# Performance work log

Hardware: AMD Instinct MI355X
Metric: run time of the kernel (lower is better)

The kernel has to match this reference:

```python
import jax, jax.numpy as jnp
import numpy as np


def _gelu(x):
    # tf.nn.gelu default is exact (erf) gelu
    return jax.nn.gelu(x, approximate=False)


def _reduce_gat(x, W, A):
    # x: [..., n, f]; W: [f, d]; A: [2d, 1]
    wx = x @ W                                   # [..., n, d]
    root = jnp.broadcast_to(wx[..., 0:1, :], wx.shape)  # gather idx 0 + repeat
    cat = jnp.concatenate([wx, root], axis=-1)   # [..., n, 2d]
    z = _gelu(cat @ A)                           # Dense(1, activation=gelu)
    att = jax.nn.softmax(_gelu(z), axis=-2)      # gelu applied twice, then softmax over n
    return _gelu(jnp.sum(wx * att, axis=-2))     # [..., d]


def _layer(x, W, A):
    # W: [H, f, d], A: [H, 2d, 1]; mean over heads
    heads = jax.vmap(lambda w, a: _reduce_gat(x, w, a))(W, A)
    return jnp.mean(heads, axis=0)


def setup_inputs() -> dict:
    key = jax.random.key(0)
    k = jax.random.split(key, 5)
    B, N2, N1, F, D, H = 512, 16, 16, 256, 256, 4
    x = jax.random.normal(k[0], (B, N2, N1, F), dtype=jnp.float32)
    W0 = jax.random.normal(k[1], (H, F, D), dtype=jnp.float32) * 0.05
    A0 = jax.random.normal(k[2], (H, 2 * D, 1), dtype=jnp.float32) * 0.05
    W1 = jax.random.normal(k[3], (H, D, D), dtype=jnp.float32) * 0.05
    A1 = jax.random.normal(k[4], (H, 2 * D, 1), dtype=jnp.float32) * 0.05
    return {"x": x, "W0": W0, "A0": A0, "W1": W1, "A1": A1}


def reference(x, W0, A0, W1, A1):
    x = _layer(x, W0, A0)  # [B, N2, D]
    x = _layer(x, W1, A1)  # [B, D]
    return x
```

## Files before the change

kernel.cpp:

```cpp
#include <hip/hip_runtime.h>
#include <math.h>

typedef _Float16 half_t;
typedef __attribute__((ext_vector_type(8))) _Float16 half8;
typedef __attribute__((ext_vector_type(16))) float floatx16;

__device__ __forceinline__ float gelu_exact(float v) {
    return 0.5f * v * (1.0f + erff(v * 0.7071067811865476f));
}

__device__ __forceinline__ floatx16 zero16() {
    floatx16 z;
#pragma unroll
    for (int i = 0; i < 16; ++i) z[i] = 0.f;
    return z;
}

__device__ __forceinline__ int swz(int b) { return b ^ (((b >> 9) & 7) << 4); }

template <bool SWZ>
__device__ __forceinline__ half8 lds_frag(const half_t* p, int byteoff) {
    if (SWZ) byteoff = swz(byteoff);
    return *(const half8*)((const char*)p + byteoff);
}

#define MFMA16(a, b, c) __builtin_amdgcn_mfma_f32_32x32x16_f16((a), (b), (c), 0, 0, 0)

__global__ __launch_bounds__(256) void prep(const float* __restrict__ W0,
                                            const float* __restrict__ A0,
                                            const float* __restrict__ W1,
                                            const float* __restrict__ A1,
                                            half_t* __restrict__ Wsw0, half_t* __restrict__ Wsw1,
                                            half_t* __restrict__ Zah0, half_t* __restrict__ Zal0,
                                            half_t* __restrict__ Zah1, half_t* __restrict__ Zal1) {
    __shared__ float tile[32][257];
    const int t  = threadIdx.x;
    const int kb = blockIdx.x & 7;
    const int h  = (blockIdx.x >> 3) & 3;
    const int tz = blockIdx.x >> 5;
    const float* W = tz ? W1 : W0;
    const float* A = tz ? A1 : A0;
    half_t* Wsw = tz ? Wsw1 : Wsw0;
    half_t* Zh  = tz ? Zah1 : Zah0;
    half_t* Zl  = tz ? Zal1 : Zal0;

    for (int i = 0; i < 32; ++i)
        tile[i][t] = W[(size_t)(h * 256 + kb * 32 + i) * 256 + t];
    __syncthreads();

    const int j = t >> 5, lmn = t & 31;
#pragma unroll
    for (int i0 = 0; i0 < 32; i0 += 8) {
        const int ks = 2 * kb + (i0 >> 4);
        const int qq = (i0 >> 3) & 1;
        half_t hb[8];
#pragma unroll
        for (int ii = 0; ii < 8; ++ii) hb[ii] = (half_t)tile[i0 + ii][t];
        size_t off = ((size_t)(h * 16 + ks) * 8 + j) * 512 + (size_t)(32 * qq + lmn) * 8;
        *(half8*)&Wsw[off] = *(half8*)hb;
    }

    if (kb == 0) {
        const float4* Wr = (const float4*)&W[(size_t)(h * 256 + t) * 256];
        const float4* Al = (const float4*)&A[h * 512];
        const float4* Ah = (const float4*)&A[h * 512 + 256];
        float wl = 0.f, wh = 0.f;
        for (int d = 0; d < 64; ++d) {
            float4 wv = Wr[d], a0 = Al[d], a1 = Ah[d];
            wl += wv.x * a0.x + wv.y * a0.y + wv.z * a0.z + wv.w * a0.w;
            wh += wv.x * a1.x + wv.y * a1.y + wv.z * a1.z + wv.w * a1.w;
        }
        half_t hi = (half_t)wl;
        Zh[(2 * h) * 256 + t] = hi;
        Zl[(2 * h) * 256 + t] = (half_t)(wl - (float)hi);
        hi = (half_t)wh;
        Zh[(2 * h + 1) * 256 + t] = hi;
        Zl[(2 * h + 1) * 256 + t] = (half_t)(wh - (float)hi);
        if (h == 0) {
            for (int c = 8; c < 32; ++c) {
                Zh[c * 256 + t] = (half_t)0.f;
                Zl[c * 256 + t] = (half_t)0.f;
            }
        }
    }
}

template <int GROUPS>
__global__ __launch_bounds__(256, 2) void gat_layer(
    const float* __restrict__ x,
    const half_t* __restrict__ Wsw,
    const half_t* __restrict__ Zah, const half_t* __restrict__ Zal,
    float* __restrict__ out) {
    constexpr int ROWS = GROUPS * 16;
    constexpr int MT   = ROWS / 32;

    __shared__ half_t xsh[MT * 16 * 512];
    __shared__ half_t xsl[MT * 16 * 512];
    __shared__ float zlo_s[4][ROWS];
    __shared__ float zhi_s[4][ROWS];
    __shared__ float ge_s[4][ROWS];
    __shared__ float att_s[4][ROWS];

    const int t  = threadIdx.x;
    const int w  = t >> 6;
    const int l  = t & 63;
    const int lm = t & 31;
    const int q  = (t >> 5) & 1;

    {
        const float4* xg = (const float4*)(x + (size_t)blockIdx.x * ROWS * 256);
#pragma unroll
        for (int i = 0; i < ROWS / 8; ++i) {
            int e = t + 256 * i;
            int row = e >> 5, cc = e & 31;
            float4 v0 = xg[row * 64 + 2 * cc];
            float4 v1 = xg[row * 64 + 2 * cc + 1];
            half_t hb[8], lb[8];
            const float* vf = &v0.x;
#pragma unroll
            for (int ii = 0; ii < 8; ++ii) {
                float v = (ii < 4) ? vf[ii] : (&v1.x)[ii - 4];
                half_t hv = (half_t)v;
                hb[ii] = hv;
                lb[ii] = (half_t)(v - (float)hv);
            }
            int m = row >> 5, r31 = row & 31, ks = cc >> 1, kq = cc & 1;
            int base = ((m * 16 + ks) * 64 + 32 * kq + r31) * 8;
            *(half8*)&xsh[base] = *(half8*)hb;
            *(half8*)&xsl[base] = *(half8*)lb;
        }
    }
    __syncthreads();

    if (w == 0) {
        floatx16 zm[MT], zc[MT];
#pragma unroll
        for (int mt = 0; mt < MT; ++mt) { zm[mt] = zero16(); zc[mt] = zero16(); }
#pragma unroll 4
        for (int ks = 0; ks < 16; ++ks) {
            const int ko = lm * 256 + 16 * ks + 8 * q;
            half8 bh = *(const half8*)&Zah[ko];
            half8 bl = *(const half8*)&Zal[ko];
#pragma unroll
            for (int mt = 0; mt < MT; ++mt) {
                half8 a  = *(const half8*)&xsh[((mt * 16 + ks) * 64 + l) * 8];
                half8 al = *(const half8*)&xsl[((mt * 16 + ks) * 64 + l) * 8];
                zm[mt] = MFMA16(a, bh, zm[mt]);
                zc[mt] = MFMA16(al, bh, zc[mt]);
                zc[mt] = MFMA16(a, bl, zc[mt]);
            }
        }
        if (lm < 8) {
            int h = lm >> 1;
            float* dst = (lm & 1) ? &zhi_s[h][0] : &zlo_s[h][0];
#pragma unroll
            for (int mt = 0; mt < MT; ++mt)
#pragma unroll
                for (int r = 0; r < 16; ++r) {
                    int row = 32 * mt + 4 * q + (r & 3) + 8 * (r >> 2);
                    dst[row] = zm[mt][r] + zc[mt][r];
                }
        }
    }
    __syncthreads();

    {
        int h = t >> 6, r = t & 63;
        if (r < ROWS) {
            float z = zlo_s[h][r] + zhi_s[h][r & ~15];
            ge_s[h][r] = gelu_exact(gelu_exact(z));
        }
    }
    __syncthreads();
    {
        int h = t >> 6, r = t & 63;
        if (r < ROWS) {
            int g0 = r & ~15;
            float mx = -1e30f;
#pragma unroll
            for (int i = 0; i < 16; ++i) mx = fmaxf(mx, ge_s[h][g0 + i]);
            float s = 0.f;
#pragma unroll
            for (int i = 0; i < 16; ++i) s += expf(ge_s[h][g0 + i] - mx);
            att_s[h][r] = expf(ge_s[h][r] - mx) / s;
        }
    }
    __syncthreads();

    float outp[2][GROUPS];
#pragma unroll
    for (int nt = 0; nt < 2; ++nt)
#pragma unroll
        for (int g = 0; g < GROUPS; ++g) outp[nt][g] = 0.f;

#pragma unroll 1
    for (int h = 0; h < 4; ++h) {
        float tp[2][GROUPS];
#pragma unroll
        for (int nt = 0; nt < 2; ++nt)
#pragma unroll
            for (int g = 0; g < GROUPS; ++g) tp[nt][g] = 0.f;

        const half_t* Bp = Wsw + ((size_t)(h * 16) * 8 + 2 * w) * 512 + (size_t)l * 8;

#pragma unroll 1
        for (int pass = 0; pass < 2; ++pass) {
            const half_t* Xp = pass ? xsl : xsh;
            floatx16 acc[MT][2];
#pragma unroll
            for (int mt = 0; mt < MT; ++mt) { acc[mt][0] = zero16(); acc[mt][1] = zero16(); }

#pragma unroll
            for (int ks = 0; ks < 16; ++ks) {
                half8 b0 = *(const half8*)(Bp + (size_t)ks * 4096);
                half8 b1 = *(const half8*)(Bp + (size_t)ks * 4096 + 512);
#pragma unroll
                for (int mt = 0; mt < MT; ++mt) {
                    half8 a = *(const half8*)&Xp[((mt * 16 + ks) * 64 + l) * 8];
                    acc[mt][0] = MFMA16(a, b0, acc[mt][0]);
                    acc[mt][1] = MFMA16(a, b1, acc[mt][1]);
                }
            }

#pragma unroll
            for (int mt = 0; mt < MT; ++mt)
#pragma unroll
                for (int k = 0; k < 4; ++k) {
                    float4 a4 = *(const float4*)&att_s[h][32 * mt + 4 * q + 8 * k];
#pragma unroll
                    for (int jj = 0; jj < 4; ++jj) {
                        int r = 4 * k + jj;
                        int row = 32 * mt + 4 * q + 8 * k + jj;
                        int g = row >> 4;
                        float av = (&a4.x)[jj];
                        tp[0][g] = fmaf(acc[mt][0][r], av, tp[0][g]);
                        tp[1][g] = fmaf(acc[mt][1][r], av, tp[1][g]);
                    }
                }
        }

#pragma unroll
        for (int nt = 0; nt < 2; ++nt)
#pragma unroll
            for (int g = 0; g < GROUPS; ++g) {
                float s = tp[nt][g] + __shfl_xor(tp[nt][g], 32, 64);
                outp[nt][g] += gelu_exact(s);
            }
    }

    if (q == 0) {
#pragma unroll
        for (int g = 0; g < GROUPS; ++g) {
            size_t ro = ((size_t)blockIdx.x * GROUPS + g) * 256 + 64 * w;
            out[ro + lm]      = 0.25f * outp[0][g];
            out[ro + 32 + lm] = 0.25f * outp[1][g];
        }
    }
}


__device__ __forceinline__ void stage_chunk(const float4* __restrict__ xg,
                                            half_t* __restrict__ xsh,
                                            half_t* __restrict__ xsl, int e) {
    int row = e >> 5, cc = e & 31;
    float4 v0 = xg[row * 64 + 2 * cc];
    float4 v1 = xg[row * 64 + 2 * cc + 1];
    half_t hb[8], lb[8];
#pragma unroll
    for (int ii = 0; ii < 8; ++ii) {
        float v = (ii < 4) ? (&v0.x)[ii] : (&v1.x)[ii - 4];
        half_t hv = (half_t)v;
        hb[ii] = hv;
        lb[ii] = (half_t)(v - (float)hv);
    }
    int base = ((cc >> 1) * 64 + 32 * (cc & 1) + row) * 16;
    *(half8*)((char*)xsh + swz(base)) = *(half8*)hb;
    *(half8*)((char*)xsl + swz(base)) = *(half8*)lb;
}

__device__ __forceinline__ void z_phase(const half_t* __restrict__ xsh,
                                        const half_t* __restrict__ xsl,
                                        const half_t* __restrict__ Zah,
                                        const half_t* __restrict__ Zal,
                                        float* __restrict__ zrow,
                                        int w, int l, int lm, int q) {
    floatx16 zp = zero16();
#pragma unroll
    for (int kk = 0; kk < 4; ++kk) {
        int ks = 4 * w + kk;
        int ko = lm * 256 + 16 * ks + 8 * q;
        half8 bh = *(const half8*)&Zah[ko];
        half8 bl = *(const half8*)&Zal[ko];
        int ao = (ks * 64 + l) * 16;
        half8 ah = lds_frag<true>(xsh, ao);
        half8 al = lds_frag<true>(xsl, ao);
        zp = MFMA16(ah, bh, zp);
        zp = MFMA16(al, bh, zp);
        zp = MFMA16(ah, bl, zp);
    }
    if (lm < 8) {
#pragma unroll
        for (int r = 0; r < 16; ++r) {
            int row = 4 * q + (r & 3) + 8 * (r >> 2);
            zrow[row * 9 + lm] = zp[r];
        }
    }
}

__global__ __launch_bounds__(512, 1) void gat2(
    const float* __restrict__ y1, const half_t* __restrict__ Wsw,
    const half_t* __restrict__ Zah, const half_t* __restrict__ Zal,
    float* __restrict__ out) {
    __shared__ __align__(16) half_t xsh[16 * 512];
    __shared__ __align__(16) half_t xsl[16 * 512];
    __shared__ float zpart[4][32][9];
    __shared__ __align__(16) float ge_s[4][32];
    __shared__ __align__(16) float att_s[4][32];
    __shared__ float outp_s[4][2][256];

    const int t = threadIdx.x;
    const int w = t >> 6, l = t & 63, lm = t & 31, q = (t >> 5) & 1;

    const float4* xg = (const float4*)(y1 + (size_t)blockIdx.x * 32 * 256);
    stage_chunk(xg, xsh, xsl, t);
    stage_chunk(xg, xsh, xsl, t + 512);
    __syncthreads();

    if (w < 4) z_phase(xsh, xsl, Zah, Zal, &zpart[w][0][0], w, l, lm, q);
    __syncthreads();

    if (t < 128) {
        int h = t >> 5, r = t & 31;
        int c0 = 2 * h, c1 = 2 * h + 1, rr = r & ~15;
        float own  = zpart[0][r][c0] + zpart[1][r][c0] + zpart[2][r][c0] + zpart[3][r][c0];
        float root = zpart[0][rr][c1] + zpart[1][rr][c1] + zpart[2][rr][c1] + zpart[3][rr][c1];
        ge_s[h][r] = gelu_exact(gelu_exact(own + root));
    }
    __syncthreads();
    if (t < 128) {
        int h = t >> 5, r = t & 31;
        int g0 = r & ~15;
        float mx = -1e30f;
#pragma unroll
        for (int i = 0; i < 16; ++i) mx = fmaxf(mx, ge_s[h][g0 + i]);
        float sum = 0.f;
#pragma unroll
        for (int i = 0; i < 16; ++i) sum += expf(ge_s[h][g0 + i] - mx);
        att_s[h][r] = expf(ge_s[h][r] - mx) / sum;
    }
    __syncthreads();

    const int h = w >> 1, s = w & 1;
    const half_t* Bp = Wsw + ((size_t)(h * 16) * 8 + 4 * s) * 512 + (size_t)l * 8;

    float tp[4][2];
#pragma unroll
    for (int jc = 0; jc < 4; ++jc) { tp[jc][0] = 0.f; tp[jc][1] = 0.f; }

#pragma unroll 1
    for (int pass = 0; pass < 2; ++pass) {
        const half_t* Xp = pass ? xsl : xsh;
        floatx16 acc[4];
#pragma unroll
        for (int jc = 0; jc < 4; ++jc) acc[jc] = zero16();
#pragma unroll
        for (int ks = 0; ks < 16; ++ks) {
            int ao = (ks * 64 + l) * 16;
            half8 a = lds_frag<true>(Xp, ao);
#pragma unroll
            for (int jc = 0; jc < 4; ++jc) {
                half8 b = *(const half8*)(Bp + (size_t)ks * 4096 + jc * 512);
                acc[jc] = MFMA16(a, b, acc[jc]);
            }
        }
#pragma unroll
        for (int g = 0; g < 2; ++g)
#pragma unroll
            for (int k2 = 0; k2 < 2; ++k2)
#pragma unroll
                for (int jj = 0; jj < 4; ++jj) {
                    float av = att_s[h][16 * g + 8 * k2 + 4 * q + jj];
                    int r = jj + 4 * k2 + 8 * g;
#pragma unroll
                    for (int jc = 0; jc < 4; ++jc)
                        tp[jc][g] = fmaf(acc[jc][r], av, tp[jc][g]);
                }
    }

#pragma unroll
    for (int g = 0; g < 2; ++g)
#pragma unroll
        for (int jc = 0; jc < 4; ++jc) {
            float sf = tp[jc][g] + __shfl_xor(tp[jc][g], 32, 64);
            if (q == 0) outp_s[h][g][128 * s + 32 * jc + lm] = gelu_exact(sf);
        }
    __syncthreads();

    {
        int g = t >> 8, col = t & 255;
        float sm = outp_s[0][g][col] + outp_s[1][g][col] + outp_s[2][g][col] + outp_s[3][g][col];
        out[((size_t)blockIdx.x * 2 + g) * 256 + col] = 0.25f * sm;
    }
}

extern "C" void kernel_launch(void* const* d_in, const int* in_sizes, int n_in,
                              void* d_out, int out_size, void* d_ws, size_t ws_size,
                              hipStream_t stream) {
    const float* x  = (const float*)d_in[0];
    const float* W0 = (const float*)d_in[1];
    const float* A0 = (const float*)d_in[2];
    const float* W1 = (const float*)d_in[3];
    const float* A1 = (const float*)d_in[4];

    char* ws = (char*)d_ws;
    float*  y1   = (float*)ws;
    half_t* Wsw0 = (half_t*)(ws + 8388608);
    half_t* Wsw1 = (half_t*)(ws + 8912896);
    half_t* Zah0 = (half_t*)(ws + 9437184);
    half_t* Zal0 = (half_t*)(ws + 9453568);
    half_t* Zah1 = (half_t*)(ws + 9469952);
    half_t* Zal1 = (half_t*)(ws + 9486336);

    prep<<<64, 256, 0, stream>>>(W0, A0, W1, A1, Wsw0, Wsw1, Zah0, Zal0, Zah1, Zal1);
    gat_layer<4><<<2048, 256, 0, stream>>>(x, Wsw0, Zah0, Zal0, y1);
    gat2<<<256, 512, 0, stream>>>(y1, Wsw1, Zah1, Zal1, (float*)d_out);
}
```

Measured before the change: 372.9 us.

## Split layer-1 across two kernels and widen gat2 to 1024 threads

Adds a gat1m kernel that processes 64 rows per block with two M-tiles, so each W fragment loaded from global memory is reused across two MFMA row tiles. Layer-1 work is split evenly: half the blocks still run the existing gat_layer kernel and half run the new one, launched back to back. gat2 now uses 1024 threads, with each wave covering a narrower N strip and doing both the high and low fp16 passes in one loop instead of two sequential passes. The aim is more reuse of weight fragments and more parallelism per block, at the cost of higher register pressure and an extra kernel launch.

```diff
diff --git a/kernel.cpp b/kernel.cpp
--- a/kernel.cpp
+++ b/kernel.cpp
@@ -18,10 +18,8 @@
 
 __device__ __forceinline__ int swz(int b) { return b ^ (((b >> 9) & 7) << 4); }
 
-template <bool SWZ>
-__device__ __forceinline__ half8 lds_frag(const half_t* p, int byteoff) {
-    if (SWZ) byteoff = swz(byteoff);
-    return *(const half8*)((const char*)p + byteoff);
+__device__ __forceinline__ half8 lds_swz(const half_t* p, int byteoff) {
+    return *(const half8*)((const char*)p + swz(byteoff));
 }
 
 #define MFMA16(a, b, c) __builtin_amdgcn_mfma_f32_32x32x16_f16((a), (b), (c), 0, 0, 0)
@@ -273,41 +271,160 @@
         hb[ii] = hv;
         lb[ii] = (half_t)(v - (float)hv);
     }
-    int base = ((cc >> 1) * 64 + 32 * (cc & 1) + row) * 16;
+    int m = row >> 5, r31 = row & 31, ks = cc >> 1, kq = cc & 1;
+    int base = ((m * 16 + ks) * 64 + 32 * kq + r31) * 16;
     *(half8*)((char*)xsh + swz(base)) = *(half8*)hb;
     *(half8*)((char*)xsl + swz(base)) = *(half8*)lb;
 }
 
+template <int MT>
 __device__ __forceinline__ void z_phase(const half_t* __restrict__ xsh,
                                         const half_t* __restrict__ xsl,
                                         const half_t* __restrict__ Zah,
                                         const half_t* __restrict__ Zal,
                                         float* __restrict__ zrow,
                                         int w, int l, int lm, int q) {
-    floatx16 zp = zero16();
+    floatx16 zp[MT];
+#pragma unroll
+    for (int mt = 0; mt < MT; ++mt) zp[mt] = zero16();
 #pragma unroll
     for (int kk = 0; kk < 4; ++kk) {
         int ks = 4 * w + kk;
         int ko = lm * 256 + 16 * ks + 8 * q;
         half8 bh = *(const half8*)&Zah[ko];
         half8 bl = *(const half8*)&Zal[ko];
-        int ao = (ks * 64 + l) * 16;
-        half8 ah = lds_frag<true>(xsh, ao);
-        half8 al = lds_frag<true>(xsl, ao);
-        zp = MFMA16(ah, bh, zp);
-        zp = MFMA16(al, bh, zp);
-        zp = MFMA16(ah, bl, zp);
+#pragma unroll
+        for (int mt = 0; mt < MT; ++mt) {
+            int ao = ((mt * 16 + ks) * 64 + l) * 16;
+            half8 ah = lds_swz(xsh, ao);
+            half8 al = lds_swz(xsl, ao);
+            zp[mt] = MFMA16(ah, bh, zp[mt]);
+            zp[mt] = MFMA16(al, bh, zp[mt]);
+            zp[mt] = MFMA16(ah, bl, zp[mt]);
+        }
     }
     if (lm < 8) {
 #pragma unroll
-        for (int r = 0; r < 16; ++r) {
-            int row = 4 * q + (r & 3) + 8 * (r >> 2);
-            zrow[row * 9 + lm] = zp[r];
-        }
-    }
-}
-
-__global__ __launch_bounds__(512, 1) void gat2(
+        for (int mt = 0; mt < MT; ++mt)
+#pragma unroll
+            for (int r = 0; r < 16; ++r) {
+                int row = 32 * mt + 4 * q + (r & 3) + 8 * (r >> 2);
+                zrow[row * 9 + lm] = zp[mt][r];
+            }
+    }
+}
+
+__global__ __launch_bounds__(256, 2) void gat1m(
+    const float* __restrict__ x, const half_t* __restrict__ Wsw,
+    const half_t* __restrict__ Zah, const half_t* __restrict__ Zal,
+    float* __restrict__ out) {
+    __shared__ __align__(16) half_t xsh[32 * 512];
+    __shared__ __align__(16) half_t xsl[32 * 512];
+    __shared__ float zpart[4][64][9];
+    __shared__ __align__(16) float ge_s[4][64];
+    __shared__ __align__(16) float att_s[4][64];
+
+    const int t = threadIdx.x;
+    const int w = t >> 6, l = t & 63, lm = t & 31, q = (t >> 5) & 1;
+
+    const float4* xg = (const float4*)(x + (size_t)blockIdx.x * 64 * 256);
+#pragma unroll
+    for (int i = 0; i < 8; ++i) stage_chunk(xg, xsh, xsl, t + 256 * i);
+    __syncthreads();
+
+    z_phase<2>(xsh, xsl, Zah, Zal, &zpart[w][0][0], w, l, lm, q);
+    __syncthreads();
+
+    {
+        int h = t >> 6, r = t & 63;
+        int c0 = 2 * h, c1 = 2 * h + 1, rr = r & ~15;
+        float own  = zpart[0][r][c0] + zpart[1][r][c0] + zpart[2][r][c0] + zpart[3][r][c0];
+        float root = zpart[0][rr][c1] + zpart[1][rr][c1] + zpart[2][rr][c1] + zpart[3][rr][c1];
+        ge_s[h][r] = gelu_exact(gelu_exact(own + root));
+    }
+    __syncthreads();
+    {
+        int h = t >> 6, r = t & 63;
+        int g0 = r & ~15;
+        float mx = -1e30f;
+#pragma unroll
+        for (int i = 0; i < 16; ++i) mx = fmaxf(mx, ge_s[h][g0 + i]);
+        float sum = 0.f;
+#pragma unroll
+        for (int i = 0; i < 16; ++i) sum += expf(ge_s[h][g0 + i] - mx);
+        att_s[h][r] = expf(ge_s[h][r] - mx) / sum;
+    }
+    __syncthreads();
+
+    float outp[2][4];
+#pragma unroll
+    for (int nt = 0; nt < 2; ++nt)
+#pragma unroll
+        for (int g = 0; g < 4; ++g) outp[nt][g] = 0.f;
+
+#pragma unroll 1
+    for (int h = 0; h < 4; ++h) {
+        const half_t* Bp = Wsw + ((size_t)(h * 16) * 8 + 2 * w) * 512 + (size_t)l * 8;
+        floatx16 acc[2][2];
+        acc[0][0] = zero16(); acc[0][1] = zero16();
+        acc[1][0] = zero16(); acc[1][1] = zero16();
+#pragma unroll
+        for (int ks = 0; ks < 16; ++ks) {
+            half8 b0 = *(const half8*)(Bp + (size_t)ks * 4096);
+            half8 b1 = *(const half8*)(Bp + (size_t)ks * 4096 + 512);
+#pragma unroll
+            for (int mt = 0; mt < 2; ++mt) {
+                int ao = ((mt * 16 + ks) * 64 + l) * 16;
+                half8 ah = lds_swz(xsh, ao);
+                half8 al = lds_swz(xsl, ao);
+                acc[mt][0] = MFMA16(ah, b0, acc[mt][0]);
+                acc[mt][0] = MFMA16(al, b0, acc[mt][0]);
+                acc[mt][1] = MFMA16(ah, b1, acc[mt][1]);
+                acc[mt][1] = MFMA16(al, b1, acc[mt][1]);
+            }
+        }
+
+        float tp[2][4];
+#pragma unroll
+        for (int nt = 0; nt < 2; ++nt)
+#pragma unroll
+            for (int g = 0; g < 4; ++g) tp[nt][g] = 0.f;
+#pragma unroll
+        for (int mt = 0; mt < 2; ++mt)
+#pragma unroll
+            for (int k2 = 0; k2 < 2; ++k2)
+#pragma unroll
+                for (int kk = 0; kk < 2; ++kk)
+#pragma unroll
+                    for (int jj = 0; jj < 4; ++jj) {
+                        const int k = 2 * k2 + kk;
+                        const int r = 4 * k + jj;
+                        const int g = 2 * mt + k2;
+                        float av = att_s[h][32 * mt + 8 * k + 4 * q + jj];
+                        tp[0][g] = fmaf(acc[mt][0][r], av, tp[0][g]);
+                        tp[1][g] = fmaf(acc[mt][1][r], av, tp[1][g]);
+                    }
+
+#pragma unroll
+        for (int nt = 0; nt < 2; ++nt)
+#pragma unroll
+            for (int g = 0; g < 4; ++g) {
+                float s = tp[nt][g] + __shfl_xor(tp[nt][g], 32, 64);
+                outp[nt][g] += gelu_exact(s);
+            }
+    }
+
+    if (q == 0) {
+#pragma unroll
+        for (int g = 0; g < 4; ++g) {
+            size_t ro = ((size_t)blockIdx.x * 4 + g) * 256 + 64 * w;
+            out[ro + lm]      = 0.25f * outp[0][g];
+            out[ro + 32 + lm] = 0.25f * outp[1][g];
+        }
+    }
+}
+
+__global__ __launch_bounds__(1024, 1) void gat2(
     const float* __restrict__ y1, const half_t* __restrict__ Wsw,
     const half_t* __restrict__ Zah, const half_t* __restrict__ Zal,
     float* __restrict__ out) {
@@ -323,10 +440,9 @@
 
     const float4* xg = (const float4*)(y1 + (size_t)blockIdx.x * 32 * 256);
     stage_chunk(xg, xsh, xsl, t);
-    stage_chunk(xg, xsh, xsl, t + 512);
-    __syncthreads();
-
-    if (w < 4) z_phase(xsh, xsl, Zah, Zal, &zpart[w][0][0], w, l, lm, q);
+    __syncthreads();
+
+    if (w < 4) z_phase<1>(xsh, xsl, Zah, Zal, &zpart[w][0][0], w, l, lm, q);
     __syncthreads();
 
     if (t < 128) {
@@ -350,56 +466,50 @@
     }
     __syncthreads();
 
-    const int h = w >> 1, s = w & 1;
-    const half_t* Bp = Wsw + ((size_t)(h * 16) * 8 + 4 * s) * 512 + (size_t)l * 8;
-
-    float tp[4][2];
-#pragma unroll
-    for (int jc = 0; jc < 4; ++jc) { tp[jc][0] = 0.f; tp[jc][1] = 0.f; }
-
-#pragma unroll 1
-    for (int pass = 0; pass < 2; ++pass) {
-        const half_t* Xp = pass ? xsl : xsh;
-        floatx16 acc[4];
-#pragma unroll
-        for (int jc = 0; jc < 4; ++jc) acc[jc] = zero16();
-#pragma unroll
-        for (int ks = 0; ks < 16; ++ks) {
-            int ao = (ks * 64 + l) * 16;
-            half8 a = lds_frag<true>(Xp, ao);
-#pragma unroll
-            for (int jc = 0; jc < 4; ++jc) {
-                half8 b = *(const half8*)(Bp + (size_t)ks * 4096 + jc * 512);
-                acc[jc] = MFMA16(a, b, acc[jc]);
-            }
-        }
-#pragma unroll
-        for (int g = 0; g < 2; ++g)
-#pragma unroll
-            for (int k2 = 0; k2 < 2; ++k2)
-#pragma unroll
-                for (int jj = 0; jj < 4; ++jj) {
-                    float av = att_s[h][16 * g + 8 * k2 + 4 * q + jj];
-                    int r = jj + 4 * k2 + 8 * g;
-#pragma unroll
-                    for (int jc = 0; jc < 4; ++jc)
-                        tp[jc][g] = fmaf(acc[jc][r], av, tp[jc][g]);
-                }
-    }
-
-#pragma unroll
-    for (int g = 0; g < 2; ++g)
-#pragma unroll
-        for (int jc = 0; jc < 4; ++jc) {
-            float sf = tp[jc][g] + __shfl_xor(tp[jc][g], 32, 64);
-            if (q == 0) outp_s[h][g][128 * s + 32 * jc + lm] = gelu_exact(sf);
-        }
-    __syncthreads();
-
-    {
+    const int head = w >> 2, strip = w & 3;
+    const half_t* Bp = Wsw + ((size_t)(head * 16) * 8 + 2 * strip) * 512 + (size_t)l * 8;
+
+    floatx16 acc0 = zero16(), acc1 = zero16();
+#pragma unroll
+    for (int ks = 0; ks < 16; ++ks) {
+        half8 b0 = *(const half8*)(Bp + (size_t)ks * 4096);
+        half8 b1 = *(const half8*)(Bp + (size_t)ks * 4096 + 512);
+        int ao = (ks * 64 + l) * 16;
+        half8 ah = lds_swz(xsh, ao);
+        half8 al = lds_swz(xsl, ao);
+        acc0 = MFMA16(ah, b0, acc0);
+        acc0 = MFMA16(al, b0, acc0);
+        acc1 = MFMA16(ah, b1, acc1);
+        acc1 = MFMA16(al, b1, acc1);
+    }
+    float tp[2][2];
+    tp[0][0] = tp[0][1] = tp[1][0] = tp[1][1] = 0.f;
+#pragma unroll
+    for (int k2 = 0; k2 < 2; ++k2)
+#pragma unroll
+        for (int kk = 0; kk < 2; ++kk)
+#pragma unroll
+            for (int jj = 0; jj < 4; ++jj) {
+                const int k = 2 * k2 + kk;
+                const int r = 4 * k + jj;
+                const int g = k2;
+                float av = att_s[head][16 * g + 8 * kk + 4 * q + jj];
+                tp[0][g] = fmaf(acc0[r], av, tp[0][g]);
+                tp[1][g] = fmaf(acc1[r], av, tp[1][g]);
+            }
+#pragma unroll
+    for (int nt = 0; nt < 2; ++nt)
+#pragma unroll
+        for (int g = 0; g < 2; ++g) {
+            float s = tp[nt][g] + __shfl_xor(tp[nt][g], 32, 64);
+            if (q == 0) outp_s[head][g][64 * strip + 32 * nt + lm] = gelu_exact(s);
+        }
+    __syncthreads();
+
+    if (t < 512) {
         int g = t >> 8, col = t & 255;
-        float sm = outp_s[0][g][col] + outp_s[1][g][col] + outp_s[2][g][col] + outp_s[3][g][col];
-        out[((size_t)blockIdx.x * 2 + g) * 256 + col] = 0.25f * sm;
+        float s = outp_s[0][g][col] + outp_s[1][g][col] + outp_s[2][g][col] + outp_s[3][g][col];
+        out[((size_t)blockIdx.x * 2 + g) * 256 + col] = 0.25f * s;
     }
 }
 
@@ -422,6 +532,8 @@
     half_t* Zal1 = (half_t*)(ws + 9486336);
 
     prep<<<64, 256, 0, stream>>>(W0, A0, W1, A1, Wsw0, Wsw1, Zah0, Zal0, Zah1, Zal1);
-    gat_layer<4><<<2048, 256, 0, stream>>>(x, Wsw0, Zah0, Zal0, y1);
-    gat2<<<256, 512, 0, stream>>>(y1, Wsw1, Zah1, Zal1, (float*)d_out);
-}
+    gat_layer<4><<<1024, 256, 0, stream>>>(x, Wsw0, Zah0, Zal0, y1);
+    gat1m<<<1024, 256, 0, stream>>>(x + (size_t)1024 * 64 * 256, Wsw0, Zah0, Zal0,
+                                    y1 + (size_t)1024 * 4 * 256);
+    gat2<<<256, 1024, 0, stream>>>(y1, Wsw1, Zah1, Zal1, (float*)d_out);
+}
```

Result: slower. 400.4 us (+7.4%).
